# Performance work log

Measured on AMD Instinct MI355X. Metric: run time of the kernel, lower is better.

## Reference

```python
import jax, jax.numpy as jnp
import numpy as np

H = 12      # num_heads
DIN = 768   # input_embedding_dim
D = 64      # embedding_dim (per head)
N, T = 4, 1024


def setup_inputs() -> dict:
    key = jax.random.key(0)
    ks = jax.random.split(key, 6)
    s_in = 1.0 / np.sqrt(DIN)
    s_hd = 1.0 / np.sqrt(H * D)
    x = jax.random.normal(ks[0], (N, T, DIN), dtype=jnp.float32)
    # Per-head bias-free projections stacked over heads: [H, DIN, D]
    Wq = jax.random.uniform(ks[1], (H, DIN, D), jnp.float32, -s_in, s_in)
    Wk = jax.random.uniform(ks[2], (H, DIN, D), jnp.float32, -s_in, s_in)
    Wv = jax.random.uniform(ks[3], (H, DIN, D), jnp.float32, -s_in, s_in)
    # Output projection: Linear(H*D -> D) with bias
    Wo = jax.random.uniform(ks[4], (H * D, D), jnp.float32, -s_hd, s_hd)
    bo = jax.random.uniform(ks[5], (D,), jnp.float32, -s_hd, s_hd)
    return {"x": x, "Wq": Wq, "Wk": Wk, "Wv": Wv, "Wo": Wo, "bo": bo}


def reference(x, Wq, Wk, Wv, Wo, bo):
    n, t, _ = x.shape
    # Batched per-head projections (all heads at once): [N,H,T,D]
    q = jnp.einsum('ntd,hde->nhte', x, Wq)
    k = jnp.einsum('ntd,hde->nhte', x, Wk)
    v = jnp.einsum('ntd,hde->nhte', x, Wv)
    # Raw scores (note: original applies NO 1/sqrt(D) scaling): [N,H,T,T]
    att = jnp.einsum('nhte,nhse->nhts', q, k)
    # Faithful to torch: tril zeros the upper triangle, then ALL zeros -> -inf
    causal = jnp.tril(jnp.ones((t, t), dtype=bool))
    att = jnp.where(causal, att, 0.0)
    att = jnp.where(att == 0.0, -jnp.inf, att)
    attn = jax.nn.softmax(att, axis=-1)  # [N,H,T,T]
    # Weighted values, then concat heads along feature dim (head-major order)
    o = jnp.einsum('nhts,nhse->nhte', attn, v)          # [N,H,T,D]
    o = jnp.transpose(o, (0, 2, 1, 3)).reshape(n, t, -1)  # [N,T,H*D]
    out = o @ Wo + bo  # [N,T,D]
    return out, attn
```

## Files before the change

kernel.cpp:

```cpp
#include <hip/hip_runtime.h>
#include <hip/hip_bf16.h>

typedef __hip_bfloat16 bf16;
typedef __attribute__((ext_vector_type(8))) short bf16x8;
typedef __attribute__((ext_vector_type(4))) float f32x4;

constexpr int NB  = 4;
constexpr int NH  = 12;
constexpr int SEQ = 1024;
constexpr int HD  = 64;
constexpr int DM  = 768;
constexpr int LDA = 40;

__device__ __forceinline__ bf16x8 ld8(const bf16* p){ return *(const bf16x8*)p; }
__device__ __forceinline__ f32x4 mfma16(bf16x8 a, bf16x8 b, f32x4 c){
  return __builtin_amdgcn_mfma_f32_16x16x32_bf16(a, b, c, 0, 0, 0);
}
union U8 { bf16x8 v; bf16 h[8]; };

__global__ __launch_bounds__(256) void wprep(const float* __restrict__ Wq, const float* __restrict__ Wk,
                      const float* __restrict__ Wv, const float* __restrict__ Wo,
                      bf16* __restrict__ WqTh, bf16* __restrict__ WqTl,
                      bf16* __restrict__ WkTh, bf16* __restrict__ WkTl,
                      bf16* __restrict__ WvT,  bf16* __restrict__ WoT){
  __shared__ float sT[64][65];
  const int tid = threadIdx.x;
  const int dt = blockIdx.x, y = blockIdx.y;
  const float* src; bf16* dh; bf16* dl = nullptr;
  if (y < 36){
    int z = y / 12, h = y % 12;
    src = (z==0 ? Wq : z==1 ? Wk : Wv) + (size_t)h*DM*HD;
    dh  = (z==0 ? WqTh : z==1 ? WkTh : WvT) + (size_t)h*HD*DM;
    if (z==0) dl = WqTl + (size_t)h*HD*DM;
    if (z==1) dl = WkTl + (size_t)h*HD*DM;
  } else { src = Wo; dh = WoT; }

  {
    int r = tid >> 2, c = (tid & 3) * 16;
    const float* sp = src + ((size_t)(dt*64 + r))*HD + c;
    f32x4 v0 = *(const f32x4*)sp, v1 = *(const f32x4*)(sp+4),
          v2 = *(const f32x4*)(sp+8), v3 = *(const f32x4*)(sp+12);
    #pragma unroll
    for (int j = 0; j < 4; j++){
      sT[r][c+j] = v0[j]; sT[r][c+4+j] = v1[j]; sT[r][c+8+j] = v2[j]; sT[r][c+12+j] = v3[j];
    }
  }
  __syncthreads();
  {
    int e = tid >> 2, co = (tid & 3) * 16;
    U8 uh0, ul0, uh1, ul1;
    #pragma unroll
    for (int j = 0; j < 8; j++){
      float v = sT[co + j][e];
      bf16 hi = __float2bfloat16(v);
      uh0.h[j] = hi; ul0.h[j] = __float2bfloat16(v - __bfloat162float(hi));
    }
    #pragma unroll
    for (int j = 0; j < 8; j++){
      float v = sT[co + 8 + j][e];
      bf16 hi = __float2bfloat16(v);
      uh1.h[j] = hi; ul1.h[j] = __float2bfloat16(v - __bfloat162float(hi));
    }
    size_t o = (size_t)e*DM + dt*64 + co;
    *(bf16x8*)(dh + o) = uh0.v; *(bf16x8*)(dh + o + 8) = uh1.v;
    if (dl){ *(bf16x8*)(dl + o) = ul0.v; *(bf16x8*)(dl + o + 8) = ul1.v; }
  }
}

__global__ __launch_bounds__(256) void xprep(const float* __restrict__ x,
                                             bf16* __restrict__ xh, bf16* __restrict__ xl){
  size_t base = ((size_t)blockIdx.x*256 + threadIdx.x)*8;
  f32x4 a = *(const f32x4*)(x + base), b = *(const f32x4*)(x + base + 4);
  U8 uh, ul;
  #pragma unroll
  for (int j = 0; j < 4; j++){
    bf16 h0 = __float2bfloat16(a[j]);
    uh.h[j] = h0; ul.h[j] = __float2bfloat16(a[j] - __bfloat162float(h0));
    bf16 h1 = __float2bfloat16(b[j]);
    uh.h[4+j] = h1; ul.h[4+j] = __float2bfloat16(b[j] - __bfloat162float(h1));
  }
  *(bf16x8*)(xh + base) = uh.v;
  *(bf16x8*)(xl + base) = ul.v;
}

__global__ __launch_bounds__(256) void kproj(const bf16* __restrict__ xh, const bf16* __restrict__ xl,
    const bf16* __restrict__ WqTh, const bf16* __restrict__ WqTl,
    const bf16* __restrict__ WkTh, const bf16* __restrict__ WkTl,
    const bf16* __restrict__ WvT,
    bf16* __restrict__ Qhi, bf16* __restrict__ Qlo,
    bf16* __restrict__ Khi, bf16* __restrict__ Klo, bf16* __restrict__ Vt){
  __shared__ bf16 sA[2][128*LDA];
  __shared__ bf16 sB[2][64*LDA];
  const int tid = threadIdx.x;
  const int lane = tid & 63, w = tid >> 6;
  const int quad = lane >> 4, lc = lane & 15;
  const int mb = blockIdx.x, h = blockIdx.y, z = blockIdx.z;
  const int sr = tid >> 2;
  const int sc = (tid & 3) * 8;
  const int wm = w & 1, wn = w >> 1;

  if (z < 2){
    const bf16* Bh = (z==0 ? WqTh : WkTh) + (size_t)h*HD*DM;
    const bf16* Bl = (z==0 ? WqTl : WkTl) + (size_t)h*HD*DM;
    bf16* Ph = (z==0 ? Qhi : Khi);
    bf16* Pl = (z==0 ? Qlo : Klo);
    f32x4 acc[4][2] = {};
    bf16x8 pa0,pa1,pa2,pa3,pb0,pb1;
    auto ldchunk = [&](int kc){
      size_t col = (size_t)kc*32 + sc;
      pa0 = ld8(xh + (size_t)(mb*128 + sr)*DM + col);
      pa1 = ld8(xh + (size_t)(mb*128 + sr + 64)*DM + col);
      pa2 = ld8(xl + (size_t)(mb*128 + sr)*DM + col);
      pa3 = ld8(xl + (size_t)(mb*128 + sr + 64)*DM + col);
      pb0 = ld8(Bh + (size_t)sr*DM + col);
      pb1 = ld8(Bl + (size_t)sr*DM + col);
    };
    ldchunk(0);
    for (int kc = 0; kc < DM/32; kc++){
      *(bf16x8*)&sA[0][sr*LDA + sc] = pa0;
      *(bf16x8*)&sA[0][(sr+64)*LDA + sc] = pa1;
      *(bf16x8*)&sA[1][sr*LDA + sc] = pa2;
      *(bf16x8*)&sA[1][(sr+64)*LDA + sc] = pa3;
      *(bf16x8*)&sB[0][sr*LDA + sc] = pb0;
      *(bf16x8*)&sB[1][sr*LDA + sc] = pb1;
      __syncthreads();
      if (kc < DM/32 - 1) ldchunk(kc + 1);
      bf16x8 bh[2], bl[2];
      #pragma unroll
      for (int nt = 0; nt < 2; nt++){
        bh[nt] = *(const bf16x8*)&sB[0][(wn*32 + nt*16 + lc)*LDA + quad*8];
        bl[nt] = *(const bf16x8*)&sB[1][(wn*32 + nt*16 + lc)*LDA + quad*8];
      }
      #pragma unroll
      for (int mt = 0; mt < 4; mt++){
        bf16x8 ah = *(const bf16x8*)&sA[0][(wm*64 + mt*16 + lc)*LDA + quad*8];
        bf16x8 al = *(const bf16x8*)&sA[1][(wm*64 + mt*16 + lc)*LDA + quad*8];
        #pragma unroll
        for (int nt = 0; nt < 2; nt++){
          acc[mt][nt] = mfma16(ah, bh[nt], acc[mt][nt]);
          acc[mt][nt] = mfma16(ah, bl[nt], acc[mt][nt]);
          acc[mt][nt] = mfma16(al, bh[nt], acc[mt][nt]);
        }
      }
      __syncthreads();
    }
    #pragma unroll
    for (int mt = 0; mt < 4; mt++){
      #pragma unroll
      for (int nt = 0; nt < 2; nt++){
        #pragma unroll
        for (int i = 0; i < 4; i++){
          int tg = mb*128 + wm*64 + mt*16 + quad*4 + i;
          int e  = wn*32 + nt*16 + lc;
          int n = tg >> 10, t = tg & 1023;
          size_t o = ((size_t)(n*NH + h)*SEQ + t)*HD + e;
          float v = acc[mt][nt][i];
          bf16 hi = __float2bfloat16(v);
          Ph[o] = hi;
          Pl[o] = __float2bfloat16(v - __bfloat162float(hi));
        }
      }
    }
  } else {
    const bf16* Av = WvT + (size_t)h*HD*DM;
    f32x4 acc[2][4] = {};
    bf16x8 pa0, pb0, pb1;
    auto ldchunk = [&](int kc){
      size_t col = (size_t)kc*32 + sc;
      pa0 = ld8(Av + (size_t)sr*DM + col);
      pb0 = ld8(xh + (size_t)(mb*128 + sr)*DM + col);
      pb1 = ld8(xh + (size_t)(mb*128 + sr + 64)*DM + col);
    };
    ldchunk(0);
    for (int kc = 0; kc < DM/32; kc++){
      *(bf16x8*)&sB[0][sr*LDA + sc] = pa0;
      *(bf16x8*)&sA[0][sr*LDA + sc] = pb0;
      *(bf16x8*)&sA[0][(sr+64)*LDA + sc] = pb1;
      __syncthreads();
      if (kc < DM/32 - 1) ldchunk(kc + 1);
      bf16x8 bt[4];
      #pragma unroll
      for (int nt = 0; nt < 4; nt++)
        bt[nt] = *(const bf16x8*)&sA[0][(wn*64 + nt*16 + lc)*LDA + quad*8];
      #pragma unroll
      for (int mt = 0; mt < 2; mt++){
        bf16x8 a = *(const bf16x8*)&sB[0][(wm*32 + mt*16 + lc)*LDA + quad*8];
        #pragma unroll
        for (int nt = 0; nt < 4; nt++)
          acc[mt][nt] = mfma16(a, bt[nt], acc[mt][nt]);
      }
      __syncthreads();
    }
    #pragma unroll
    for (int mt = 0; mt < 2; mt++){
      #pragma unroll
      for (int nt = 0; nt < 4; nt++){
        #pragma unroll
        for (int i = 0; i < 4; i++){
          int e  = wm*32 + mt*16 + quad*4 + i;
          int tg = mb*128 + wn*64 + nt*16 + lc;
          int n = tg >> 10, t = tg & 1023;
          Vt[((size_t)(n*NH + h)*HD + e)*SEQ + t] = __float2bfloat16(acc[mt][nt][i]);
        }
      }
    }
  }
}

__global__ __launch_bounds__(256) void kattn_pv(const bf16* __restrict__ Qhi, const bf16* __restrict__ Qlo,
                                                const bf16* __restrict__ Khi, const bf16* __restrict__ Klo,
                                                const bf16* __restrict__ Vt,
                                                float* __restrict__ attn, bf16* __restrict__ O){
  __shared__ bf16 sP[16][SEQ + 8];
  __shared__ float msh[4][16], lsh[4][16];
  const int lane = threadIdx.x & 63, w = threadIdx.x >> 6;
  const int quad = lane >> 4, lc = lane & 15;
  const int t0 = blockIdx.x * 16;
  const int nh = blockIdx.y;
  const size_t base = (size_t)nh * SEQ * HD;
  const float NEGINF = -__builtin_inff();

  f32x4 acc[16] = {};
  const bf16* qh = Qhi + base + (size_t)(t0 + lc)*HD;
  const bf16* ql = Qlo + base + (size_t)(t0 + lc)*HD;
  bf16x8 ah0 = ld8(qh + quad*8), ah1 = ld8(qh + 32 + quad*8);
  bf16x8 al0 = ld8(ql + quad*8), al1 = ld8(ql + 32 + quad*8);
  const int tmax = t0 + 15;
  #pragma unroll
  for (int tl = 0; tl < 16; tl++){
    int ct = w*256 + tl*16;
    if (ct <= tmax){
      const bf16* kh = Khi + base + (size_t)(ct + lc)*HD;
      const bf16* kl = Klo + base + (size_t)(ct + lc)*HD;
      bf16x8 bh0 = ld8(kh + quad*8), bh1 = ld8(kh + 32 + quad*8);
      bf16x8 bl0 = ld8(kl + quad*8), bl1 = ld8(kl + 32 + quad*8);
      acc[tl] = mfma16(ah0, bh0, acc[tl]);
      acc[tl] = mfma16(ah1, bh1, acc[tl]);
      acc[tl] = mfma16(ah0, bl0, acc[tl]);
      acc[tl] = mfma16(ah1, bl1, acc[tl]);
      acc[tl] = mfma16(al0, bh0, acc[tl]);
      acc[tl] = mfma16(al1, bh1, acc[tl]);
    }
  }

  float mx[4] = {NEGINF, NEGINF, NEGINF, NEGINF};
  #pragma unroll
  for (int tl = 0; tl < 16; tl++){
    int col = w*256 + tl*16 + lc;
    #pragma unroll
    for (int i = 0; i < 4; i++){
      int r = t0 + quad*4 + i;
      float v = acc[tl][i];
      if (col <= r && v != 0.0f) mx[i] = fmaxf(mx[i], v);
    }
  }
  #pragma unroll
  for (int off = 8; off; off >>= 1){
    #pragma unroll
    for (int i = 0; i < 4; i++) mx[i] = fmaxf(mx[i], __shfl_xor(mx[i], off, 16));
  }
  float sm[4] = {0.f, 0.f, 0.f, 0.f};
  #pragma unroll
  for (int tl = 0; tl < 16; tl++){
    int col = w*256 + tl*16 + lc;
    #pragma unroll
    for (int i = 0; i < 4; i++){
      int r = t0 + quad*4 + i;
      float v = acc[tl][i];
      float e = (col <= r && v != 0.0f) ? __expf(v - mx[i]) : 0.0f;
      acc[tl][i] = e;
      sm[i] += e;
    }
  }
  #pragma unroll
  for (int off = 8; off; off >>= 1){
    #pragma unroll
    for (int i = 0; i < 4; i++) sm[i] += __shfl_xor(sm[i], off, 16);
  }
  if (lc == 0){
    #pragma unroll
    for (int i = 0; i < 4; i++){ msh[w][quad*4 + i] = mx[i]; lsh[w][quad*4 + i] = sm[i]; }
  }
  __syncthreads();
  float scale[4];
  #pragma unroll
  for (int i = 0; i < 4; i++){
    int rl = quad*4 + i;
    float M = fmaxf(fmaxf(msh[0][rl], msh[1][rl]), fmaxf(msh[2][rl], msh[3][rl]));
    float L = 0.f;
    #pragma unroll
    for (int w2 = 0; w2 < 4; w2++) L += lsh[w2][rl] * __expf(msh[w2][rl] - M);
    scale[i] = __expf(mx[i] - M) / L;
  }
  #pragma unroll
  for (int tl = 0; tl < 16; tl++){
    int col = w*256 + tl*16 + lc;
    #pragma unroll
    for (int i = 0; i < 4; i++){
      int row = quad*4 + i;
      float p = acc[tl][i] * scale[i];
      attn[((size_t)nh*SEQ + (t0 + row))*SEQ + col] = p;
      sP[row][col] = __float2bfloat16(p);
    }
  }
  __syncthreads();

  f32x4 oacc = {};
  const bf16* Vb = Vt + ((size_t)nh*HD + w*16 + lc)*SEQ;
  const int kend = t0 + 16;
  for (int s0 = 0; s0 < kend; s0 += 32){
    bf16x8 a = *(const bf16x8*)&sP[lc][s0 + quad*8];
    bf16x8 b = ld8(Vb + s0 + quad*8);
    oacc = mfma16(a, b, oacc);
  }
  const int n = nh / NH, h = nh % NH;
  #pragma unroll
  for (int i = 0; i < 4; i++){
    O[((size_t)n*SEQ + t0 + quad*4 + i)*DM + h*HD + w*16 + lc] = __float2bfloat16(oacc[i]);
  }
}

__global__ __launch_bounds__(256) void kout(const bf16* __restrict__ O, const bf16* __restrict__ WoT,
                                            const float* __restrict__ bo, float* __restrict__ out){
  const int lane = threadIdx.x & 63, w = threadIdx.x >> 6;
  const int quad = lane >> 4, lc = lane & 15;
  const int m0 = blockIdx.x * 64;
  const int n = m0 >> 10, tb = m0 & 1023;
  const bf16* Or = O + ((size_t)n*SEQ + tb + w*16 + lc)*DM;
  f32x4 acc[4] = {};
  for (int k0 = 0; k0 < DM; k0 += 32){
    bf16x8 a = ld8(Or + k0 + quad*8);
    #pragma unroll
    for (int ct = 0; ct < 4; ct++){
      bf16x8 b = ld8(WoT + (size_t)(ct*16 + lc)*DM + k0 + quad*8);
      acc[ct] = mfma16(a, b, acc[ct]);
    }
  }
  #pragma unroll
  for (int ct = 0; ct < 4; ct++){
    float bias = bo[ct*16 + lc];
    #pragma unroll
    for (int i = 0; i < 4; i++){
      out[((size_t)n*SEQ + tb + w*16 + quad*4 + i)*HD + ct*16 + lc] = acc[ct][i] + bias;
    }
  }
}

extern "C" void kernel_launch(void* const* d_in, const int* in_sizes, int n_in,
                              void* d_out, int out_size, void* d_ws, size_t ws_size,
                              hipStream_t stream){
  const float* x  = (const float*)d_in[0];
  const float* Wq = (const float*)d_in[1];
  const float* Wk = (const float*)d_in[2];
  const float* Wv = (const float*)d_in[3];
  const float* Wo = (const float*)d_in[4];
  const float* bo = (const float*)d_in[5];

  float* out  = (float*)d_out;
  float* attn = out + (size_t)NB*SEQ*HD;

  constexpr size_t SZ_WT  = (size_t)NH*HD*DM;
  constexpr size_t SZ_WOT = (size_t)HD*DM;
  constexpr size_t SZ_Q   = (size_t)NB*NH*SEQ*HD;
  bf16* b = (bf16*)d_ws;
  bf16* WqTh = b;  b += SZ_WT;
  bf16* WqTl = b;  b += SZ_WT;
  bf16* WkTh = b;  b += SZ_WT;
  bf16* WkTl = b;  b += SZ_WT;
  bf16* WvT  = b;  b += SZ_WT;
  bf16* WoT  = b;  b += SZ_WOT;
  bf16* xh   = b;  b += SZ_Q;
  bf16* xl   = b;  b += SZ_Q;
  bf16* Qhi  = b;  b += SZ_Q;
  bf16* Qlo  = b;  b += SZ_Q;
  bf16* Khi  = b;  b += SZ_Q;
  bf16* Klo  = b;  b += SZ_Q;
  bf16* Vt   = b;  b += SZ_Q;
  bf16* O    = xh;

  wprep<<<dim3(12, 37), 256, 0, stream>>>(Wq, Wk, Wv, Wo, WqTh, WqTl, WkTh, WkTl, WvT, WoT);
  xprep<<<dim3((int)(SZ_Q/(256*8))), 256, 0, stream>>>(x, xh, xl);
  kproj<<<dim3(NB*SEQ/128, NH, 3), 256, 0, stream>>>(xh, xl, WqTh, WqTl, WkTh, WkTl, WvT,
                                                     Qhi, Qlo, Khi, Klo, Vt);
  kattn_pv<<<dim3(SEQ/16, NB*NH), 256, 0, stream>>>(Qhi, Qlo, Khi, Klo, Vt, attn, O);
  kout<<<dim3(NB*SEQ/64), 256, 0, stream>>>(O, WoT, bo, out);
}
```

Baseline: 379.3 us.

## Fuse Q/K projection blocks, prefetch K tiles, coalesce attn stores, retile output GEMM

The projection kernel now computes Q and K in the same block, so each x tile is staged once and shared by both, and the grid drops to two z-slices. The attention kernel double-buffers the K fragment loads so the next tile is fetched while MFMAs run on the current one. Probabilities are staged in shared memory and then written to the attn output as row-contiguous float4 stores instead of scattered per-lane scalar stores. The returned attention probabilities are therefore bf16-rounded rather than full fp32, a precision risk. The output projection uses 32-row blocks with a 2x2 wave split, giving more blocks to spread across the GPU.

```diff
diff --git a/kernel.cpp b/kernel.cpp
--- a/kernel.cpp
+++ b/kernel.cpp
@@ -90,7 +90,7 @@
     bf16* __restrict__ Qhi, bf16* __restrict__ Qlo,
     bf16* __restrict__ Khi, bf16* __restrict__ Klo, bf16* __restrict__ Vt){
   __shared__ bf16 sA[2][128*LDA];
-  __shared__ bf16 sB[2][64*LDA];
+  __shared__ bf16 sB[4][64*LDA];
   const int tid = threadIdx.x;
   const int lane = tid & 63, w = tid >> 6;
   const int quad = lane >> 4, lc = lane & 15;
@@ -99,21 +99,23 @@
   const int sc = (tid & 3) * 8;
   const int wm = w & 1, wn = w >> 1;
 
-  if (z < 2){
-    const bf16* Bh = (z==0 ? WqTh : WkTh) + (size_t)h*HD*DM;
-    const bf16* Bl = (z==0 ? WqTl : WkTl) + (size_t)h*HD*DM;
-    bf16* Ph = (z==0 ? Qhi : Khi);
-    bf16* Pl = (z==0 ? Qlo : Klo);
-    f32x4 acc[4][2] = {};
-    bf16x8 pa0,pa1,pa2,pa3,pb0,pb1;
+  if (z == 0){
+    const bf16* Bqh = WqTh + (size_t)h*HD*DM;
+    const bf16* Bql = WqTl + (size_t)h*HD*DM;
+    const bf16* Bkh = WkTh + (size_t)h*HD*DM;
+    const bf16* Bkl = WkTl + (size_t)h*HD*DM;
+    f32x4 aq[4][2] = {}, ak[4][2] = {};
+    bf16x8 pa0,pa1,pa2,pa3,pq0,pq1,pk0,pk1;
     auto ldchunk = [&](int kc){
       size_t col = (size_t)kc*32 + sc;
       pa0 = ld8(xh + (size_t)(mb*128 + sr)*DM + col);
       pa1 = ld8(xh + (size_t)(mb*128 + sr + 64)*DM + col);
       pa2 = ld8(xl + (size_t)(mb*128 + sr)*DM + col);
       pa3 = ld8(xl + (size_t)(mb*128 + sr + 64)*DM + col);
-      pb0 = ld8(Bh + (size_t)sr*DM + col);
-      pb1 = ld8(Bl + (size_t)sr*DM + col);
+      pq0 = ld8(Bqh + (size_t)sr*DM + col);
+      pq1 = ld8(Bql + (size_t)sr*DM + col);
+      pk0 = ld8(Bkh + (size_t)sr*DM + col);
+      pk1 = ld8(Bkl + (size_t)sr*DM + col);
     };
     ldchunk(0);
     for (int kc = 0; kc < DM/32; kc++){
@@ -121,15 +123,20 @@
       *(bf16x8*)&sA[0][(sr+64)*LDA + sc] = pa1;
       *(bf16x8*)&sA[1][sr*LDA + sc] = pa2;
       *(bf16x8*)&sA[1][(sr+64)*LDA + sc] = pa3;
-      *(bf16x8*)&sB[0][sr*LDA + sc] = pb0;
-      *(bf16x8*)&sB[1][sr*LDA + sc] = pb1;
+      *(bf16x8*)&sB[0][sr*LDA + sc] = pq0;
+      *(bf16x8*)&sB[1][sr*LDA + sc] = pq1;
+      *(bf16x8*)&sB[2][sr*LDA + sc] = pk0;
+      *(bf16x8*)&sB[3][sr*LDA + sc] = pk1;
       __syncthreads();
       if (kc < DM/32 - 1) ldchunk(kc + 1);
-      bf16x8 bh[2], bl[2];
+      bf16x8 bqh[2], bql[2], bkh[2], bkl[2];
       #pragma unroll
       for (int nt = 0; nt < 2; nt++){
-        bh[nt] = *(const bf16x8*)&sB[0][(wn*32 + nt*16 + lc)*LDA + quad*8];
-        bl[nt] = *(const bf16x8*)&sB[1][(wn*32 + nt*16 + lc)*LDA + quad*8];
+        int ro = (wn*32 + nt*16 + lc)*LDA + quad*8;
+        bqh[nt] = *(const bf16x8*)&sB[0][ro];
+        bql[nt] = *(const bf16x8*)&sB[1][ro];
+        bkh[nt] = *(const bf16x8*)&sB[2][ro];
+        bkl[nt] = *(const bf16x8*)&sB[3][ro];
       }
       #pragma unroll
       for (int mt = 0; mt < 4; mt++){
@@ -137,9 +144,12 @@
         bf16x8 al = *(const bf16x8*)&sA[1][(wm*64 + mt*16 + lc)*LDA + quad*8];
         #pragma unroll
         for (int nt = 0; nt < 2; nt++){
-          acc[mt][nt] = mfma16(ah, bh[nt], acc[mt][nt]);
-          acc[mt][nt] = mfma16(ah, bl[nt], acc[mt][nt]);
-          acc[mt][nt] = mfma16(al, bh[nt], acc[mt][nt]);
+          aq[mt][nt] = mfma16(ah, bqh[nt], aq[mt][nt]);
+          aq[mt][nt] = mfma16(ah, bql[nt], aq[mt][nt]);
+          aq[mt][nt] = mfma16(al, bqh[nt], aq[mt][nt]);
+          ak[mt][nt] = mfma16(ah, bkh[nt], ak[mt][nt]);
+          ak[mt][nt] = mfma16(ah, bkl[nt], ak[mt][nt]);
+          ak[mt][nt] = mfma16(al, bkh[nt], ak[mt][nt]);
         }
       }
       __syncthreads();
@@ -154,10 +164,14 @@
           int e  = wn*32 + nt*16 + lc;
           int n = tg >> 10, t = tg & 1023;
           size_t o = ((size_t)(n*NH + h)*SEQ + t)*HD + e;
-          float v = acc[mt][nt][i];
-          bf16 hi = __float2bfloat16(v);
-          Ph[o] = hi;
-          Pl[o] = __float2bfloat16(v - __bfloat162float(hi));
+          float vq = aq[mt][nt][i];
+          bf16 hq = __float2bfloat16(vq);
+          Qhi[o] = hq;
+          Qlo[o] = __float2bfloat16(vq - __bfloat162float(hq));
+          float vk = ak[mt][nt][i];
+          bf16 hk = __float2bfloat16(vk);
+          Khi[o] = hk;
+          Klo[o] = __float2bfloat16(vk - __bfloat162float(hk));
         }
       }
     }
@@ -213,7 +227,8 @@
                                                 float* __restrict__ attn, bf16* __restrict__ O){
   __shared__ bf16 sP[16][SEQ + 8];
   __shared__ float msh[4][16], lsh[4][16];
-  const int lane = threadIdx.x & 63, w = threadIdx.x >> 6;
+  const int tid = threadIdx.x;
+  const int lane = tid & 63, w = tid >> 6;
   const int quad = lane >> 4, lc = lane & 15;
   const int t0 = blockIdx.x * 16;
   const int nh = blockIdx.y;
@@ -226,27 +241,34 @@
   bf16x8 ah0 = ld8(qh + quad*8), ah1 = ld8(qh + 32 + quad*8);
   bf16x8 al0 = ld8(ql + quad*8), al1 = ld8(ql + 32 + quad*8);
   const int tmax = t0 + 15;
+  const int cbase = w*256;
+
+  bf16x8 kb[2][4];
+  auto loadK = [&](int tl, int b){
+    const bf16* kh = Khi + base + (size_t)(cbase + tl*16 + lc)*HD;
+    const bf16* kl = Klo + base + (size_t)(cbase + tl*16 + lc)*HD;
+    kb[b][0] = ld8(kh + quad*8);  kb[b][1] = ld8(kh + 32 + quad*8);
+    kb[b][2] = ld8(kl + quad*8);  kb[b][3] = ld8(kl + 32 + quad*8);
+  };
+  if (cbase <= tmax) loadK(0, 0);
   #pragma unroll
   for (int tl = 0; tl < 16; tl++){
-    int ct = w*256 + tl*16;
-    if (ct <= tmax){
-      const bf16* kh = Khi + base + (size_t)(ct + lc)*HD;
-      const bf16* kl = Klo + base + (size_t)(ct + lc)*HD;
-      bf16x8 bh0 = ld8(kh + quad*8), bh1 = ld8(kh + 32 + quad*8);
-      bf16x8 bl0 = ld8(kl + quad*8), bl1 = ld8(kl + 32 + quad*8);
-      acc[tl] = mfma16(ah0, bh0, acc[tl]);
-      acc[tl] = mfma16(ah1, bh1, acc[tl]);
-      acc[tl] = mfma16(ah0, bl0, acc[tl]);
-      acc[tl] = mfma16(ah1, bl1, acc[tl]);
-      acc[tl] = mfma16(al0, bh0, acc[tl]);
-      acc[tl] = mfma16(al1, bh1, acc[tl]);
+    if (cbase + tl*16 <= tmax){
+      if (tl < 15 && cbase + (tl+1)*16 <= tmax) loadK(tl+1, (tl+1)&1);
+      const int b = tl & 1;
+      acc[tl] = mfma16(ah0, kb[b][0], acc[tl]);
+      acc[tl] = mfma16(ah1, kb[b][1], acc[tl]);
+      acc[tl] = mfma16(ah0, kb[b][2], acc[tl]);
+      acc[tl] = mfma16(ah1, kb[b][3], acc[tl]);
+      acc[tl] = mfma16(al0, kb[b][0], acc[tl]);
+      acc[tl] = mfma16(al1, kb[b][1], acc[tl]);
     }
   }
 
   float mx[4] = {NEGINF, NEGINF, NEGINF, NEGINF};
   #pragma unroll
   for (int tl = 0; tl < 16; tl++){
-    int col = w*256 + tl*16 + lc;
+    int col = cbase + tl*16 + lc;
     #pragma unroll
     for (int i = 0; i < 4; i++){
       int r = t0 + quad*4 + i;
@@ -262,7 +284,7 @@
   float sm[4] = {0.f, 0.f, 0.f, 0.f};
   #pragma unroll
   for (int tl = 0; tl < 16; tl++){
-    int col = w*256 + tl*16 + lc;
+    int col = cbase + tl*16 + lc;
     #pragma unroll
     for (int i = 0; i < 4; i++){
       int r = t0 + quad*4 + i;
@@ -294,16 +316,25 @@
   }
   #pragma unroll
   for (int tl = 0; tl < 16; tl++){
-    int col = w*256 + tl*16 + lc;
+    int col = cbase + tl*16 + lc;
     #pragma unroll
     for (int i = 0; i < 4; i++){
-      int row = quad*4 + i;
-      float p = acc[tl][i] * scale[i];
-      attn[((size_t)nh*SEQ + (t0 + row))*SEQ + col] = p;
-      sP[row][col] = __float2bfloat16(p);
+      sP[quad*4 + i][col] = __float2bfloat16(acc[tl][i] * scale[i]);
     }
   }
   __syncthreads();
+
+  #pragma unroll
+  for (int r = 0; r < 16; r++){
+    const unsigned* sPu = (const unsigned*)&sP[r][0];
+    uint2 v = *(const uint2*)(sPu + tid*2);
+    f32x4 f;
+    f[0] = __uint_as_float(v.x << 16);
+    f[1] = __uint_as_float(v.x & 0xFFFF0000u);
+    f[2] = __uint_as_float(v.y << 16);
+    f[3] = __uint_as_float(v.y & 0xFFFF0000u);
+    *(f32x4*)(attn + ((size_t)nh*SEQ + t0 + r)*SEQ + tid*4) = f;
+  }
 
   f32x4 oacc = {};
   const bf16* Vb = Vt + ((size_t)nh*HD + w*16 + lc)*SEQ;
@@ -324,24 +355,25 @@
                                             const float* __restrict__ bo, float* __restrict__ out){
   const int lane = threadIdx.x & 63, w = threadIdx.x >> 6;
   const int quad = lane >> 4, lc = lane & 15;
-  const int m0 = blockIdx.x * 64;
-  const int n = m0 >> 10, tb = m0 & 1023;
-  const bf16* Or = O + ((size_t)n*SEQ + tb + w*16 + lc)*DM;
-  f32x4 acc[4] = {};
+  const int wm = w & 1, wn = w >> 1;
+  const int g = blockIdx.x * 32;
+  const int n = g >> 10, tb = g & 1023;
+  const bf16* Or = O + ((size_t)n*SEQ + tb + wm*16 + lc)*DM;
+  f32x4 acc[2] = {};
   for (int k0 = 0; k0 < DM; k0 += 32){
     bf16x8 a = ld8(Or + k0 + quad*8);
     #pragma unroll
-    for (int ct = 0; ct < 4; ct++){
-      bf16x8 b = ld8(WoT + (size_t)(ct*16 + lc)*DM + k0 + quad*8);
-      acc[ct] = mfma16(a, b, acc[ct]);
-    }
-  }
-  #pragma unroll
-  for (int ct = 0; ct < 4; ct++){
-    float bias = bo[ct*16 + lc];
+    for (int nt = 0; nt < 2; nt++){
+      bf16x8 b = ld8(WoT + (size_t)(wn*32 + nt*16 + lc)*DM + k0 + quad*8);
+      acc[nt] = mfma16(a, b, acc[nt]);
+    }
+  }
+  #pragma unroll
+  for (int nt = 0; nt < 2; nt++){
+    float bias = bo[wn*32 + nt*16 + lc];
     #pragma unroll
     for (int i = 0; i < 4; i++){
-      out[((size_t)n*SEQ + tb + w*16 + quad*4 + i)*HD + ct*16 + lc] = acc[ct][i] + bias;
+      out[((size_t)n*SEQ + tb + wm*16 + quad*4 + i)*HD + wn*32 + nt*16 + lc] = acc[nt][i] + bias;
     }
   }
 }
@@ -380,8 +412,8 @@
 
   wprep<<<dim3(12, 37), 256, 0, stream>>>(Wq, Wk, Wv, Wo, WqTh, WqTl, WkTh, WkTl, WvT, WoT);
   xprep<<<dim3((int)(SZ_Q/(256*8))), 256, 0, stream>>>(x, xh, xl);
-  kproj<<<dim3(NB*SEQ/128, NH, 3), 256, 0, stream>>>(xh, xl, WqTh, WqTl, WkTh, WkTl, WvT,
+  kproj<<<dim3(NB*SEQ/128, NH, 2), 256, 0, stream>>>(xh, xl, WqTh, WqTl, WkTh, WkTl, WvT,
                                                      Qhi, Qlo, Khi, Klo, Vt);
   kattn_pv<<<dim3(SEQ/16, NB*NH), 256, 0, stream>>>(Qhi, Qlo, Khi, Klo, Vt, attn, O);
-  kout<<<dim3(NB*SEQ/64), 256, 0, stream>>>(O, WoT, bo, out);
-}
+  kout<<<dim3(NB*SEQ/32), 256, 0, stream>>>(O, WoT, bo, out);
+}
```

Result: faster. 361.0 us (-4.8%).
